# Performance work log

Hardware: AMD Instinct MI355X
Metric: run time of the kernel (lower is better)

Reference implementation:

```python
import jax, jax.numpy as jnp
import numpy as np

LAYERS = 3
DILATION = 2
RES_NORM = 1.0 / np.sqrt(2.0).astype(np.float32)
NEG_SLOPE = 0.2
T, B, D = 256, 128, 1024


def setup_inputs() -> dict:
    key = jax.random.key(0)
    k0, k1, k2, k3, k4 = jax.random.split(key, 5)
    s = 1.0 / np.sqrt(D)  # torch GRUCell default init bound
    x = jax.random.normal(k0, (1, T, B, D), dtype=jnp.float32)
    W_ih = jax.random.uniform(k1, (LAYERS, 3 * D, D), jnp.float32, -s, s)
    W_hh = jax.random.uniform(k2, (LAYERS, 3 * D, D), jnp.float32, -s, s)
    b_ih = jax.random.uniform(k3, (LAYERS, 3 * D), jnp.float32, -s, s)
    b_hh = jax.random.uniform(k4, (LAYERS, 3 * D), jnp.float32, -s, s)
    return {"x": x, "W_ih": W_ih, "W_hh": W_hh, "b_ih": b_ih, "b_hh": b_hh}


def _gru_cell(x, h, W_ih, W_hh, b_ih, b_hh):
    # torch.nn.GRUCell math
    gi = x @ W_ih.T + b_ih  # [B, 3D]
    gh = h @ W_hh.T + b_hh  # [B, 3D]
    i_r, i_z, i_n = jnp.split(gi, 3, axis=-1)
    h_r, h_z, h_n = jnp.split(gh, 3, axis=-1)
    r = jax.nn.sigmoid(i_r + h_r)
    z = jax.nn.sigmoid(i_z + h_z)
    n = jnp.tanh(i_n + r * h_n)
    return (1.0 - z) * n + z * h


def reference(x, W_ih, W_hh, b_ih, b_hh):
    xs = x[0]  # squeeze(0) -> [T, B, D]
    b, d = xs.shape[1], xs.shape[2]
    # dilated hidden buffers: layer l keeps DILATION**l past hiddens (init None -> zeros)
    bufs0 = tuple(jnp.zeros((DILATION ** l, b, d), xs.dtype) for l in range(LAYERS))

    def step(bufs, x_t):
        h_in = x_t
        new_bufs = []
        for l in range(LAYERS):
            h_out = _gru_cell(h_in, bufs[l][0], W_ih[l], W_hh[l], b_ih[l], b_hh[l])
            # append h_out, pop oldest (roll buffer)
            new_bufs.append(jnp.concatenate([bufs[l][1:], h_out[None]], axis=0))
            # layers > 1 -> dilated residual + LeakyReLU(0.2), scaled by 1/sqrt(2)
            h_in = jax.nn.leaky_relu((h_out + h_in) * RES_NORM, negative_slope=NEG_SLOPE)
        return tuple(new_bufs), h_in

    _, outs = jax.lax.scan(step, bufs0, xs)  # outs: [T, B, D]
    return outs[None]  # unsqueeze(0) -> [1, T, B, D]
```

## Files before the change

### kernel.cpp

```cpp
#include <hip/hip_runtime.h>
#include <hip/hip_bf16.h>

#define TT 256
#define D 1024
#define BD (128 * 1024)
#define NWPL 85
#define NWG 256
#define NUSED 255
#define ROWLEN 1048

typedef __attribute__((ext_vector_type(8))) short bf16x8;
typedef __attribute__((ext_vector_type(4))) float f32x4;

__device__ __forceinline__ unsigned short f2bf(float f) {
    __hip_bfloat16 h = __float2bfloat16(f);
    return *reinterpret_cast<unsigned short*>(&h);
}
__device__ __forceinline__ float bf2f(unsigned short u) {
    unsigned v = (unsigned)u << 16;
    return __builtin_bit_cast(float, v);
}

__global__ __launch_bounds__(256) void cvt_f32_bf16(const float* __restrict__ in,
                                                    unsigned short* __restrict__ out, int n) {
    int i = (blockIdx.x * 256 + threadIdx.x) * 8;
    if (i + 8 <= n) {
        float4 a = *(const float4*)(in + i);
        float4 b = *(const float4*)(in + i + 4);
        unsigned short t[8] = { f2bf(a.x), f2bf(a.y), f2bf(a.z), f2bf(a.w),
                                f2bf(b.x), f2bf(b.y), f2bf(b.z), f2bf(b.w) };
        *(uint4*)(out + i) = *(const uint4*)t;
    }
}

__global__ __launch_bounds__(256, 1) void dgru_dataflow(
    const unsigned short* __restrict__ xbf,
    const float* __restrict__ Wih, const float* __restrict__ Whh,
    const float* __restrict__ bih, const float* __restrict__ bhh,
    unsigned short* __restrict__ ring_bf, float* __restrict__ ring_f,
    unsigned short* __restrict__ hin_ring,
    float* __restrict__ out,
    unsigned* __restrict__ prog)
{
    __shared__ unsigned short wlds[78 * ROWLEN];

    const int grp = blockIdx.x & 7;
    const int p = 32 * grp + (blockIdx.x >> 3);
    if (p >= NUSED) return;
    const int layer = p / NWPL;
    const int u     = p % NWPL;
    const int ncols = (u < 4) ? 13 : 12;
    const int c0    = u * 12 + (u < 4 ? u : 4);

    {
        const float* w0 = Wih + (size_t)layer * 3 * D * D;
        const float* w1 = Whh + (size_t)layer * 3 * D * D;
        const int nrows = 6 * ncols;
        for (int rid = 0; rid < nrows; ++rid) {
            int m   = rid / (3 * ncols);
            int rem = rid - m * 3 * ncols;
            int g   = rem / ncols;
            int c   = rem - g * ncols;
            const float* src = (m ? w1 : w0) + ((size_t)g * D + c0 + c) * D + threadIdx.x * 4;
            float4 v = *(const float4*)src;
            ushort4 o = { f2bf(v.x), f2bf(v.y), f2bf(v.z), f2bf(v.w) };
            *(ushort4*)&wlds[rid * ROWLEN + threadIdx.x * 4] = o;
        }
        __syncthreads();
    }

    const int tid  = threadIdx.x;
    const int wave = tid >> 6;
    const int lane = tid & 63;
    const int r15  = lane & 15;
    const int kq   = lane >> 4;
    const int kq8  = kq * 8;
    const int c_cl = (r15 < ncols) ? r15 : (ncols - 1);
    const bool cvalid = r15 < ncols;
    const int col  = c0 + c_cl;

    const float bi2 = bih[layer * 3 * D + 2 * D + col];
    const float bh2 = bhh[layer * 3 * D + 2 * D + col];
    const float bs0 = bih[layer * 3 * D + col] + bhh[layer * 3 * D + col];
    const float bs1 = bih[layer * 3 * D + D + col] + bhh[layer * 3 * D + D + col];

    const unsigned short* bp[6];
    #pragma unroll
    for (int mg = 0; mg < 6; ++mg) bp[mg] = wlds + (mg * ncols + c_cl) * ROWLEN;

    const int arow_off0 = (wave * 32 + r15) * D;
    const int arow_off1 = (wave * 32 + 16 + r15) * D;

    const int dil = 1 << layer;
    const int R   = 2 << layer;
    const int rb  = (layer == 0) ? 0 : (layer == 1 ? 2 : 6);

    unsigned* pr0 = prog;
    unsigned* pr1 = prog + 128;
    unsigned* pr2 = prog + 256;
    unsigned* myflag = prog + layer * 128 + u;

    unsigned *a1, *a2, *a3;
    if (layer == 0)      { a1 = pr0; a2 = pr1; a3 = pr2; }
    else if (layer == 1) { a1 = pr0; a2 = pr1; a3 = pr2; }
    else                 { a1 = pr1; a2 = pr2; a3 = pr2; }

    const int j2 = (lane < 21) ? lane + 64 : lane;

    for (int t = 0; t < TT; ++t) {
        int th1, th2, th3;
        if (layer == 0)      { th1 = t;     th2 = t - 7; th3 = 0; }
        else if (layer == 1) { th1 = t + 1; th2 = t - 1; th3 = t - 7; }
        else                 { th1 = t + 1; th2 = t - 3; th3 = 0; }

        if (wave == 0) {
            for (;;) {
                bool ok = true;
                if (th1 > 0) ok = ok && (int)__hip_atomic_load(a1 + lane, __ATOMIC_RELAXED, __HIP_MEMORY_SCOPE_AGENT) >= th1
                                     && (int)__hip_atomic_load(a1 + j2,   __ATOMIC_RELAXED, __HIP_MEMORY_SCOPE_AGENT) >= th1;
                if (th2 > 0) ok = ok && (int)__hip_atomic_load(a2 + lane, __ATOMIC_RELAXED, __HIP_MEMORY_SCOPE_AGENT) >= th2
                                     && (int)__hip_atomic_load(a2 + j2,   __ATOMIC_RELAXED, __HIP_MEMORY_SCOPE_AGENT) >= th2;
                if (th3 > 0) ok = ok && (int)__hip_atomic_load(a3 + lane, __ATOMIC_RELAXED, __HIP_MEMORY_SCOPE_AGENT) >= th3
                                     && (int)__hip_atomic_load(a3 + j2,   __ATOMIC_RELAXED, __HIP_MEMORY_SCOPE_AGENT) >= th3;
                if (__all(ok)) break;
                __builtin_amdgcn_s_sleep(1);
            }
            __builtin_amdgcn_fence(__ATOMIC_ACQUIRE, "agent");
        }
        __syncthreads();

        const unsigned short* hinb = layer ? hin_ring + (size_t)((layer - 1) * 8 + (t & 7)) * BD
                                           : xbf + (size_t)t * BD;
        const int rs = (t + dil) % R, wsl = t % R;
        const unsigned short* hprevb = ring_bf + (size_t)(rb + rs) * BD;
        const float*  hprevf = ring_f + (size_t)(rb + rs) * BD;
        float*        houtf  = ring_f + (size_t)(rb + wsl) * BD;
        unsigned short* houtb = ring_bf + (size_t)(rb + wsl) * BD;

        float hpv[8], rsv[8];
        #pragma unroll
        for (int rtl = 0; rtl < 2; ++rtl)
            #pragma unroll
            for (int q = 0; q < 4; ++q) {
                const int row = wave * 32 + rtl * 16 + kq * 4 + q;
                const size_t idx = (size_t)row * D + col;
                hpv[rtl * 4 + q] = hprevf[idx];
                rsv[rtl * 4 + q] = bf2f(hinb[idx]);
            }

        f32x4 acc[2][2][3] = {};
        bf16x8 A0[16], A1[16], A2[16];

#define ISSUE1(Av, KS, SL) { \
        Av[(SL) * 4 + 0] = *(const bf16x8*)(hinb   + arow_off0 + (KS) * 32 + kq8); \
        Av[(SL) * 4 + 1] = *(const bf16x8*)(hprevb + arow_off0 + (KS) * 32 + kq8); \
        Av[(SL) * 4 + 2] = *(const bf16x8*)(hinb   + arow_off1 + (KS) * 32 + kq8); \
        Av[(SL) * 4 + 3] = *(const bf16x8*)(hprevb + arow_off1 + (KS) * 32 + kq8); }
#define ISSUEG(Av, BASE) { ISSUE1(Av, (BASE) + 0, 0) ISSUE1(Av, (BASE) + 1, 1) \
                           ISSUE1(Av, (BASE) + 2, 2) ISSUE1(Av, (BASE) + 3, 3) \
                           __builtin_amdgcn_sched_barrier(0); }
#define COMPG(Av, BASE) { _Pragma("unroll") for (int kk = 0; kk < 4; ++kk) { \
        bf16x8 Bv[6]; \
        _Pragma("unroll") for (int mg = 0; mg < 6; ++mg) \
            Bv[mg] = *(const bf16x8*)(bp[mg] + ((BASE) + kk) * 32 + kq8); \
        _Pragma("unroll") for (int g = 0; g < 3; ++g) { \
            acc[0][0][g] = __builtin_amdgcn_mfma_f32_16x16x32_bf16(Av[kk * 4 + 0], Bv[g],     acc[0][0][g], 0, 0, 0); \
            acc[0][1][g] = __builtin_amdgcn_mfma_f32_16x16x32_bf16(Av[kk * 4 + 1], Bv[3 + g], acc[0][1][g], 0, 0, 0); \
            acc[1][0][g] = __builtin_amdgcn_mfma_f32_16x16x32_bf16(Av[kk * 4 + 2], Bv[g],     acc[1][0][g], 0, 0, 0); \
            acc[1][1][g] = __builtin_amdgcn_mfma_f32_16x16x32_bf16(Av[kk * 4 + 3], Bv[3 + g], acc[1][1][g], 0, 0, 0); } } \
        __builtin_amdgcn_sched_barrier(0); }

        ISSUEG(A0, 0);  ISSUEG(A1, 4);  ISSUEG(A2, 8);
        COMPG(A0, 0);   ISSUEG(A0, 12);
        COMPG(A1, 4);   ISSUEG(A1, 16);
        COMPG(A2, 8);   ISSUEG(A2, 20);
        COMPG(A0, 12);  ISSUEG(A0, 24);
        COMPG(A1, 16);  ISSUEG(A1, 28);
        COMPG(A2, 20);
        COMPG(A0, 24);
        COMPG(A1, 28);

        #pragma unroll
        for (int rtl = 0; rtl < 2; ++rtl) {
            #pragma unroll
            for (int q = 0; q < 4; ++q) {
                const int row = wave * 32 + rtl * 16 + kq * 4 + q;
                const size_t idx = (size_t)row * D + col;
                float xr = acc[rtl][0][0][q] + acc[rtl][1][0][q] + bs0;
                float xz = acc[rtl][0][1][q] + acc[rtl][1][1][q] + bs1;
                float rg = 1.f / (1.f + __expf(-xr));
                float zg = 1.f / (1.f + __expf(-xz));
                float ng = tanhf(acc[rtl][0][2][q] + bi2 + rg * (acc[rtl][1][2][q] + bh2));
                float hp = hpv[rtl * 4 + q];
                float h  = (1.f - zg) * ng + zg * hp;
                float v = (h + rsv[rtl * 4 + q]) * 0.70710678f;
                float y = v > 0.f ? v : 0.2f * v;
                if (cvalid) {
                    __hip_atomic_store(&houtf[idx], h, __ATOMIC_RELAXED, __HIP_MEMORY_SCOPE_AGENT);
                    __hip_atomic_store(&houtb[idx], f2bf(h), __ATOMIC_RELAXED, __HIP_MEMORY_SCOPE_AGENT);
                    if (layer == 2) {
                        __hip_atomic_store(&out[(size_t)t * BD + idx], y, __ATOMIC_RELAXED, __HIP_MEMORY_SCOPE_AGENT);
                    } else {
                        __hip_atomic_store(&hin_ring[(size_t)(layer * 8 + (t & 7)) * BD + idx],
                                           f2bf(y), __ATOMIC_RELAXED, __HIP_MEMORY_SCOPE_AGENT);
                    }
                }
            }
        }

        __syncthreads();
        if (tid == 0) {
            __builtin_amdgcn_fence(__ATOMIC_RELEASE, "agent");
            __hip_atomic_store(myflag, (unsigned)(t + 1), __ATOMIC_RELAXED, __HIP_MEMORY_SCOPE_AGENT);
        }
    }
}

extern "C" void kernel_launch(void* const* d_in, const int* in_sizes, int n_in,
                              void* d_out, int out_size, void* d_ws, size_t ws_size,
                              hipStream_t stream) {
    const float* x   = (const float*)d_in[0];
    const float* Wih = (const float*)d_in[1];
    const float* Whh = (const float*)d_in[2];
    const float* bih = (const float*)d_in[3];
    const float* bhh = (const float*)d_in[4];
    float* out = (float*)d_out;

    char* ws = (char*)d_ws;
    size_t off = 0;
    auto alloc = [&](size_t bytes) -> void* {
        void* p = ws + off;
        off += (bytes + 255) & ~(size_t)255;
        return p;
    };

    const int NX = TT * BD;
    unsigned short* xbf = (unsigned short*)alloc((size_t)NX * 2);

    size_t zstart = off;
    unsigned short* ring_bf  = (unsigned short*)alloc((size_t)14 * BD * 2);
    float*          ring_f   = (float*)alloc((size_t)14 * BD * 4);
    unsigned short* hin_ring = (unsigned short*)alloc((size_t)16 * BD * 2);
    unsigned*       prog     = (unsigned*)alloc(2048);
    size_t zbytes = off - zstart;

    cvt_f32_bf16<<<NX / 8 / 256, 256, 0, stream>>>(x, xbf, NX);
    hipMemsetAsync(ws + zstart, 0, zbytes, stream);

    dgru_dataflow<<<NWG, 256, 0, stream>>>(
        xbf, Wih, Whh, bih, bhh,
        ring_bf, ring_f, hin_ring, out,
        prog);
}
```

Before: 6.001 ms.

## Restructure persistent GRU kernel to stream weights from global with LDS-staged activations

The kernel moves from 255 workgroups that each keep a bf16 weight slice resident in LDS to 96 workgroups, each owning 64 output columns by 64 batch rows of one layer. Weights are now pre-converted to bf16 once and streamed from global/L2 every timestep, while activations are staged through double-buffered LDS in 128-wide K chunks. Input x is read as fp32 and converted on the fly instead of pre-converted, and the progress-flag polling now covers 32 producers per layer. This cuts the number of synchronising blocks and the flag traffic, but each step now has to pull the full 12 MB bf16 weight set through L2 with far fewer compute units.

```diff
diff --git a/kernel.cpp b/kernel.cpp
--- a/kernel.cpp
+++ b/kernel.cpp
@@ -4,13 +4,12 @@
 #define TT 256
 #define D 1024
 #define BD (128 * 1024)
-#define NWPL 85
-#define NWG 256
-#define NUSED 255
-#define ROWLEN 1048
+#define CHUNK 128
+#define APAD 136
 
 typedef __attribute__((ext_vector_type(8))) short bf16x8;
 typedef __attribute__((ext_vector_type(4))) float f32x4;
+typedef unsigned long long ull;
 
 __device__ __forceinline__ unsigned short f2bf(float f) {
     __hip_bfloat16 h = __float2bfloat16(f);
@@ -33,185 +32,215 @@
     }
 }
 
-__global__ __launch_bounds__(256, 1) void dgru_dataflow(
-    const unsigned short* __restrict__ xbf,
-    const float* __restrict__ Wih, const float* __restrict__ Whh,
+#define MF(a, b, c) __builtin_amdgcn_mfma_f32_16x16x32_bf16(a, b, c, 0, 0, 0)
+#define SB __builtin_amdgcn_sched_barrier(0)
+#define AGLD(p) __hip_atomic_load((p), __ATOMIC_RELAXED, __HIP_MEMORY_SCOPE_AGENT)
+#define AGST(p, v) __hip_atomic_store((p), (v), __ATOMIC_RELAXED, __HIP_MEMORY_SCOPE_AGENT)
+#define LBAR { SB; asm volatile("s_waitcnt lgkmcnt(0)"); __builtin_amdgcn_s_barrier(); SB; }
+
+#define STAGE_ISSUE(KC) { \
+    if (layer == 0) { \
+        _Pragma("unroll") for (int i_ = 0; i_ < 8; ++i_) { \
+            float4 v_ = *(const float4*)(xsrc + (KC) * CHUNK + i_ * 4); \
+            Sh[i_] = (ull)f2bf(v_.x) | ((ull)f2bf(v_.y) << 16) | \
+                     ((ull)f2bf(v_.z) << 32) | ((ull)f2bf(v_.w) << 48); \
+        } \
+    } else { \
+        _Pragma("unroll") for (int i_ = 0; i_ < 8; ++i_) \
+            Sh[i_] = AGLD(hsrc + (KC) * 32 + i_); \
+    } \
+    _Pragma("unroll") for (int i_ = 0; i_ < 8; ++i_) \
+        Sp[i_] = AGLD(psrc + (KC) * 32 + i_); \
+    SB; }
+
+#define STAGE_WRITE(BUF) { \
+    _Pragma("unroll") for (int i_ = 0; i_ < 4; ++i_) { \
+        uint4 wv_; \
+        wv_.x = (unsigned)Sh[i_ * 2];     wv_.y = (unsigned)(Sh[i_ * 2] >> 32); \
+        wv_.z = (unsigned)Sh[i_ * 2 + 1]; wv_.w = (unsigned)(Sh[i_ * 2 + 1] >> 32); \
+        *(uint4*)&sA[BUF][0][srow][skp + i_ * 8] = wv_; \
+        uint4 pv_; \
+        pv_.x = (unsigned)Sp[i_ * 2];     pv_.y = (unsigned)(Sp[i_ * 2] >> 32); \
+        pv_.z = (unsigned)Sp[i_ * 2 + 1]; pv_.w = (unsigned)(Sp[i_ * 2 + 1] >> 32); \
+        *(uint4*)&sA[BUF][1][srow][skp + i_ * 8] = pv_; \
+    } SB; }
+
+#define WISSUE(W, KG) { \
+    const int ko_ = (KG) * 32; \
+    _Pragma("unroll") for (int m_ = 0; m_ < 6; ++m_) { \
+        W[m_ * 2 + 0] = *(const bf16x8*)(msrc[m_] + vcol0 + ko_); \
+        W[m_ * 2 + 1] = *(const bf16x8*)(msrc[m_] + vcol1 + ko_); \
+    } SB; }
+
+#define COMP(BUF, KSL, W) { \
+    bf16x8 a00 = *(const bf16x8*)&sA[BUF][0][wrow +  0 + r15][(KSL) * 32 + kq8]; \
+    bf16x8 a01 = *(const bf16x8*)&sA[BUF][1][wrow +  0 + r15][(KSL) * 32 + kq8]; \
+    bf16x8 a10 = *(const bf16x8*)&sA[BUF][0][wrow + 16 + r15][(KSL) * 32 + kq8]; \
+    bf16x8 a11 = *(const bf16x8*)&sA[BUF][1][wrow + 16 + r15][(KSL) * 32 + kq8]; \
+    _Pragma("unroll") for (int m_ = 0; m_ < 3; ++m_) { \
+        acc[0][0][m_] = MF(a00, W[m_ * 2 + 0], acc[0][0][m_]); \
+        acc[0][1][m_] = MF(a00, W[m_ * 2 + 1], acc[0][1][m_]); \
+        acc[1][0][m_] = MF(a10, W[m_ * 2 + 0], acc[1][0][m_]); \
+        acc[1][1][m_] = MF(a10, W[m_ * 2 + 1], acc[1][1][m_]); } \
+    _Pragma("unroll") for (int m_ = 3; m_ < 6; ++m_) { \
+        acc[0][0][m_] = MF(a01, W[m_ * 2 + 0], acc[0][0][m_]); \
+        acc[0][1][m_] = MF(a01, W[m_ * 2 + 1], acc[0][1][m_]); \
+        acc[1][0][m_] = MF(a11, W[m_ * 2 + 0], acc[1][0][m_]); \
+        acc[1][1][m_] = MF(a11, W[m_ * 2 + 1], acc[1][1][m_]); } \
+    SB; }
+
+#define EPI_ISSUE { \
+    _Pragma("unroll") for (int ct_ = 0; ct_ < 2; ++ct_) \
+    _Pragma("unroll") for (int rt_ = 0; rt_ < 2; ++rt_) \
+    _Pragma("unroll") for (int q_ = 0; q_ < 4; ++q_) { \
+        const size_t idx_ = (size_t)(rbase + wrow + rt_ * 16 + kq * 4 + q_) * D + \
+                            (c0 + wcol + ct_ * 16 + r15); \
+        hpv[ct_][rt_][q_] = AGLD(hprevf + idx_); \
+        if (layer == 0) rsl0[ct_][rt_][q_] = xt[idx_]; \
+        else rpk[ct_][rt_][q_] = AGLD((const unsigned*)(hinb + (idx_ & ~(size_t)1))); \
+    } SB; }
+
+__global__ __launch_bounds__(256, 1) void dgru3(
+    const float* __restrict__ xf,
+    const unsigned short* __restrict__ Wih_bf, const unsigned short* __restrict__ Whh_bf,
     const float* __restrict__ bih, const float* __restrict__ bhh,
     unsigned short* __restrict__ ring_bf, float* __restrict__ ring_f,
-    unsigned short* __restrict__ hin_ring,
-    float* __restrict__ out,
+    unsigned short* __restrict__ hin_ring, float* __restrict__ out,
     unsigned* __restrict__ prog)
 {
-    __shared__ unsigned short wlds[78 * ROWLEN];
-
-    const int grp = blockIdx.x & 7;
-    const int p = 32 * grp + (blockIdx.x >> 3);
-    if (p >= NUSED) return;
-    const int layer = p / NWPL;
-    const int u     = p % NWPL;
-    const int ncols = (u < 4) ? 13 : 12;
-    const int c0    = u * 12 + (u < 4 ? u : 4);
-
-    {
-        const float* w0 = Wih + (size_t)layer * 3 * D * D;
-        const float* w1 = Whh + (size_t)layer * 3 * D * D;
-        const int nrows = 6 * ncols;
-        for (int rid = 0; rid < nrows; ++rid) {
-            int m   = rid / (3 * ncols);
-            int rem = rid - m * 3 * ncols;
-            int g   = rem / ncols;
-            int c   = rem - g * ncols;
-            const float* src = (m ? w1 : w0) + ((size_t)g * D + c0 + c) * D + threadIdx.x * 4;
-            float4 v = *(const float4*)src;
-            ushort4 o = { f2bf(v.x), f2bf(v.y), f2bf(v.z), f2bf(v.w) };
-            *(ushort4*)&wlds[rid * ROWLEN + threadIdx.x * 4] = o;
-        }
-        __syncthreads();
+    __shared__ __align__(16) unsigned short sA[2][2][64][APAD];
+
+    const int b = blockIdx.x;
+    const int half  = b / 48;
+    const int p     = b % 48;
+    const int j     = p >> 3;
+    const int layer = j >> 1;
+    const int slice = (j & 1) * 8 + (p & 7);
+    const int c0    = slice * 64;
+    const int myidx = slice * 2 + half;
+    const int rbase = half * 64;
+
+    const int tid = threadIdx.x;
+    const int wave = tid >> 6, lane = tid & 63;
+    const int r15 = lane & 15, kq = lane >> 4, kq8 = kq * 8;
+    const int wrow = (wave >> 1) * 32;
+    const int wcol = (wave & 1) * 32;
+
+    const unsigned short* Wl_ih = Wih_bf + (size_t)layer * 3 * D * D;
+    const unsigned short* Wl_hh = Whh_bf + (size_t)layer * 3 * D * D;
+    const unsigned short* msrc[6] = { Wl_ih, Wl_ih + D * D, Wl_ih + 2 * D * D,
+                                      Wl_hh, Wl_hh + D * D, Wl_hh + 2 * D * D };
+    const int vcol0 = (c0 + wcol + r15) * D + kq8;
+    const int vcol1 = vcol0 + 16 * D;
+
+    float bs0[2], bs1[2], bi2c[2], bh2c[2];
+    #pragma unroll
+    for (int ct = 0; ct < 2; ++ct) {
+        const int col = c0 + wcol + ct * 16 + r15;
+        bs0[ct]  = bih[layer * 3 * D + col] + bhh[layer * 3 * D + col];
+        bs1[ct]  = bih[layer * 3 * D + D + col] + bhh[layer * 3 * D + D + col];
+        bi2c[ct] = bih[layer * 3 * D + 2 * D + col];
+        bh2c[ct] = bhh[layer * 3 * D + 2 * D + col];
     }
 
-    const int tid  = threadIdx.x;
-    const int wave = tid >> 6;
-    const int lane = tid & 63;
-    const int r15  = lane & 15;
-    const int kq   = lane >> 4;
-    const int kq8  = kq * 8;
-    const int c_cl = (r15 < ncols) ? r15 : (ncols - 1);
-    const bool cvalid = r15 < ncols;
-    const int col  = c0 + c_cl;
-
-    const float bi2 = bih[layer * 3 * D + 2 * D + col];
-    const float bh2 = bhh[layer * 3 * D + 2 * D + col];
-    const float bs0 = bih[layer * 3 * D + col] + bhh[layer * 3 * D + col];
-    const float bs1 = bih[layer * 3 * D + D + col] + bhh[layer * 3 * D + D + col];
-
-    const unsigned short* bp[6];
-    #pragma unroll
-    for (int mg = 0; mg < 6; ++mg) bp[mg] = wlds + (mg * ncols + c_cl) * ROWLEN;
-
-    const int arow_off0 = (wave * 32 + r15) * D;
-    const int arow_off1 = (wave * 32 + 16 + r15) * D;
-
-    const int dil = 1 << layer;
-    const int R   = 2 << layer;
-    const int rb  = (layer == 0) ? 0 : (layer == 1 ? 2 : 6);
+    const int srow = tid >> 2;
+    const int skp  = (tid & 3) * 32;
+    const int sgoff = (rbase + srow) * D + skp;
+
+    const int dil = 1 << layer, R = 2 << layer;
+    const int rb = (layer == 0) ? 0 : (layer == 1) ? 2 : 6;
 
     unsigned* pr0 = prog;
-    unsigned* pr1 = prog + 128;
-    unsigned* pr2 = prog + 256;
-    unsigned* myflag = prog + layer * 128 + u;
-
-    unsigned *a1, *a2, *a3;
-    if (layer == 0)      { a1 = pr0; a2 = pr1; a3 = pr2; }
-    else if (layer == 1) { a1 = pr0; a2 = pr1; a3 = pr2; }
-    else                 { a1 = pr1; a2 = pr2; a3 = pr2; }
-
-    const int j2 = (lane < 21) ? lane + 64 : lane;
+    unsigned* pr1 = prog + 64;
+    unsigned* pr2 = prog + 128;
+    unsigned* myflag = prog + layer * 64 + myidx;
+    const bool oddc = (r15 & 1);
 
     for (int t = 0; t < TT; ++t) {
-        int th1, th2, th3;
-        if (layer == 0)      { th1 = t;     th2 = t - 7; th3 = 0; }
-        else if (layer == 1) { th1 = t + 1; th2 = t - 1; th3 = t - 7; }
-        else                 { th1 = t + 1; th2 = t - 3; th3 = 0; }
-
+        int th1, th2, th3; unsigned *a1, *a2, *a3;
+        if (layer == 0)      { a1 = pr0; th1 = t;     a2 = pr1; th2 = t - 7; a3 = pr2; th3 = 0;     }
+        else if (layer == 1) { a1 = pr0; th1 = t + 1; a2 = pr1; th2 = t - 1; a3 = pr2; th3 = t - 7; }
+        else                 { a1 = pr1; th1 = t + 1; a2 = pr2; th2 = t - 3; a3 = pr2; th3 = 0;     }
         if (wave == 0) {
+            const int fi = lane & 31;
             for (;;) {
                 bool ok = true;
-                if (th1 > 0) ok = ok && (int)__hip_atomic_load(a1 + lane, __ATOMIC_RELAXED, __HIP_MEMORY_SCOPE_AGENT) >= th1
-                                     && (int)__hip_atomic_load(a1 + j2,   __ATOMIC_RELAXED, __HIP_MEMORY_SCOPE_AGENT) >= th1;
-                if (th2 > 0) ok = ok && (int)__hip_atomic_load(a2 + lane, __ATOMIC_RELAXED, __HIP_MEMORY_SCOPE_AGENT) >= th2
-                                     && (int)__hip_atomic_load(a2 + j2,   __ATOMIC_RELAXED, __HIP_MEMORY_SCOPE_AGENT) >= th2;
-                if (th3 > 0) ok = ok && (int)__hip_atomic_load(a3 + lane, __ATOMIC_RELAXED, __HIP_MEMORY_SCOPE_AGENT) >= th3
-                                     && (int)__hip_atomic_load(a3 + j2,   __ATOMIC_RELAXED, __HIP_MEMORY_SCOPE_AGENT) >= th3;
+                if (th1 > 0) ok = ok && (int)AGLD(a1 + fi) >= th1;
+                if (th2 > 0) ok = ok && (int)AGLD(a2 + fi) >= th2;
+                if (th3 > 0) ok = ok && (int)AGLD(a3 + fi) >= th3;
                 if (__all(ok)) break;
                 __builtin_amdgcn_s_sleep(1);
             }
-            __builtin_amdgcn_fence(__ATOMIC_ACQUIRE, "agent");
         }
         __syncthreads();
 
-        const unsigned short* hinb = layer ? hin_ring + (size_t)((layer - 1) * 8 + (t & 7)) * BD
-                                           : xbf + (size_t)t * BD;
+        const unsigned short* hinb = hin_ring + (size_t)((layer - 1) * 8 + (t & 7)) * BD;
+        const float* xt = xf + (size_t)t * BD;
         const int rs = (t + dil) % R, wsl = t % R;
         const unsigned short* hprevb = ring_bf + (size_t)(rb + rs) * BD;
-        const float*  hprevf = ring_f + (size_t)(rb + rs) * BD;
-        float*        houtf  = ring_f + (size_t)(rb + wsl) * BD;
+        const float* hprevf = ring_f + (size_t)(rb + rs) * BD;
+        float* houtf = ring_f + (size_t)(rb + wsl) * BD;
         unsigned short* houtb = ring_bf + (size_t)(rb + wsl) * BD;
 
-        float hpv[8], rsv[8];
+        const ull* psrc = (const ull*)(hprevb + sgoff);
+        const ull* hsrc = (layer == 0) ? (const ull*)0 : (const ull*)(hinb + sgoff);
+        const float* xsrc = xt + sgoff;
+
+        ull Sh[8], Sp[8];
+        f32x4 acc[2][2][6] = {};
+        bf16x8 W0[12], W1[12];
+        float hpv[2][2][4]; unsigned rpk[2][2][4]; float rsl0[2][2][4];
+
+        STAGE_ISSUE(0);
+        STAGE_WRITE(0); LBAR;
+        WISSUE(W0, 0);
+        #pragma unroll 1
+        for (int kc = 0; kc < 8; ++kc) {
+            const int buf = kc & 1, k4 = kc * 4;
+            if (kc < 7) { STAGE_ISSUE(kc + 1); }
+            else        { EPI_ISSUE; }
+            WISSUE(W1, k4 + 1); COMP(buf, 0, W0);
+            WISSUE(W0, k4 + 2); COMP(buf, 1, W1);
+            WISSUE(W1, k4 + 3); COMP(buf, 2, W0);
+            if (kc < 7) {
+                WISSUE(W0, k4 + 4); COMP(buf, 3, W1);
+                STAGE_WRITE(buf ^ 1); LBAR;
+            } else {
+                COMP(buf, 3, W1);
+            }
+        }
+
         #pragma unroll
-        for (int rtl = 0; rtl < 2; ++rtl)
-            #pragma unroll
-            for (int q = 0; q < 4; ++q) {
-                const int row = wave * 32 + rtl * 16 + kq * 4 + q;
-                const size_t idx = (size_t)row * D + col;
-                hpv[rtl * 4 + q] = hprevf[idx];
-                rsv[rtl * 4 + q] = bf2f(hinb[idx]);
-            }
-
-        f32x4 acc[2][2][3] = {};
-        bf16x8 A0[16], A1[16], A2[16];
-
-#define ISSUE1(Av, KS, SL) { \
-        Av[(SL) * 4 + 0] = *(const bf16x8*)(hinb   + arow_off0 + (KS) * 32 + kq8); \
-        Av[(SL) * 4 + 1] = *(const bf16x8*)(hprevb + arow_off0 + (KS) * 32 + kq8); \
-        Av[(SL) * 4 + 2] = *(const bf16x8*)(hinb   + arow_off1 + (KS) * 32 + kq8); \
-        Av[(SL) * 4 + 3] = *(const bf16x8*)(hprevb + arow_off1 + (KS) * 32 + kq8); }
-#define ISSUEG(Av, BASE) { ISSUE1(Av, (BASE) + 0, 0) ISSUE1(Av, (BASE) + 1, 1) \
-                           ISSUE1(Av, (BASE) + 2, 2) ISSUE1(Av, (BASE) + 3, 3) \
-                           __builtin_amdgcn_sched_barrier(0); }
-#define COMPG(Av, BASE) { _Pragma("unroll") for (int kk = 0; kk < 4; ++kk) { \
-        bf16x8 Bv[6]; \
-        _Pragma("unroll") for (int mg = 0; mg < 6; ++mg) \
-            Bv[mg] = *(const bf16x8*)(bp[mg] + ((BASE) + kk) * 32 + kq8); \
-        _Pragma("unroll") for (int g = 0; g < 3; ++g) { \
-            acc[0][0][g] = __builtin_amdgcn_mfma_f32_16x16x32_bf16(Av[kk * 4 + 0], Bv[g],     acc[0][0][g], 0, 0, 0); \
-            acc[0][1][g] = __builtin_amdgcn_mfma_f32_16x16x32_bf16(Av[kk * 4 + 1], Bv[3 + g], acc[0][1][g], 0, 0, 0); \
-            acc[1][0][g] = __builtin_amdgcn_mfma_f32_16x16x32_bf16(Av[kk * 4 + 2], Bv[g],     acc[1][0][g], 0, 0, 0); \
-            acc[1][1][g] = __builtin_amdgcn_mfma_f32_16x16x32_bf16(Av[kk * 4 + 3], Bv[3 + g], acc[1][1][g], 0, 0, 0); } } \
-        __builtin_amdgcn_sched_barrier(0); }
-
-        ISSUEG(A0, 0);  ISSUEG(A1, 4);  ISSUEG(A2, 8);
-        COMPG(A0, 0);   ISSUEG(A0, 12);
-        COMPG(A1, 4);   ISSUEG(A1, 16);
-        COMPG(A2, 8);   ISSUEG(A2, 20);
-        COMPG(A0, 12);  ISSUEG(A0, 24);
-        COMPG(A1, 16);  ISSUEG(A1, 28);
-        COMPG(A2, 20);
-        COMPG(A0, 24);
-        COMPG(A1, 28);
-
+        for (int ct = 0; ct < 2; ++ct)
         #pragma unroll
-        for (int rtl = 0; rtl < 2; ++rtl) {
-            #pragma unroll
-            for (int q = 0; q < 4; ++q) {
-                const int row = wave * 32 + rtl * 16 + kq * 4 + q;
-                const size_t idx = (size_t)row * D + col;
-                float xr = acc[rtl][0][0][q] + acc[rtl][1][0][q] + bs0;
-                float xz = acc[rtl][0][1][q] + acc[rtl][1][1][q] + bs1;
-                float rg = 1.f / (1.f + __expf(-xr));
-                float zg = 1.f / (1.f + __expf(-xz));
-                float ng = tanhf(acc[rtl][0][2][q] + bi2 + rg * (acc[rtl][1][2][q] + bh2));
-                float hp = hpv[rtl * 4 + q];
-                float h  = (1.f - zg) * ng + zg * hp;
-                float v = (h + rsv[rtl * 4 + q]) * 0.70710678f;
-                float y = v > 0.f ? v : 0.2f * v;
-                if (cvalid) {
-                    __hip_atomic_store(&houtf[idx], h, __ATOMIC_RELAXED, __HIP_MEMORY_SCOPE_AGENT);
-                    __hip_atomic_store(&houtb[idx], f2bf(h), __ATOMIC_RELAXED, __HIP_MEMORY_SCOPE_AGENT);
-                    if (layer == 2) {
-                        __hip_atomic_store(&out[(size_t)t * BD + idx], y, __ATOMIC_RELAXED, __HIP_MEMORY_SCOPE_AGENT);
-                    } else {
-                        __hip_atomic_store(&hin_ring[(size_t)(layer * 8 + (t & 7)) * BD + idx],
-                                           f2bf(y), __ATOMIC_RELAXED, __HIP_MEMORY_SCOPE_AGENT);
-                    }
-                }
-            }
-        }
-
+        for (int rt = 0; rt < 2; ++rt)
+        #pragma unroll
+        for (int q = 0; q < 4; ++q) {
+            const size_t idx = (size_t)(rbase + wrow + rt * 16 + kq * 4 + q) * D +
+                               (c0 + wcol + ct * 16 + r15);
+            float xr = acc[rt][ct][0][q] + acc[rt][ct][3][q] + bs0[ct];
+            float xz = acc[rt][ct][1][q] + acc[rt][ct][4][q] + bs1[ct];
+            float rg = 1.f / (1.f + __expf(-xr));
+            float zg = 1.f / (1.f + __expf(-xz));
+            float ng = tanhf(acc[rt][ct][2][q] + bi2c[ct] + rg * (acc[rt][ct][5][q] + bh2c[ct]));
+            float hp = hpv[ct][rt][q];
+            float h  = (1.f - zg) * ng + zg * hp;
+            float res = (layer == 0) ? rsl0[ct][rt][q]
+                        : bf2f((unsigned short)(oddc ? (rpk[ct][rt][q] >> 16)
+                                                     : (rpk[ct][rt][q] & 0xffffu)));
+            float v = (h + res) * 0.70710678f;
+            float y = v > 0.f ? v : 0.2f * v;
+            AGST(&houtf[idx], h);
+            AGST(&houtb[idx], f2bf(h));
+            if (layer == 2) AGST(&out[(size_t)t * BD + idx], y);
+            else            AGST(&hin_ring[(size_t)(layer * 8 + (t & 7)) * BD + idx], f2bf(y));
+        }
+
+        asm volatile("s_waitcnt vmcnt(0)");
         __syncthreads();
         if (tid == 0) {
             __builtin_amdgcn_fence(__ATOMIC_RELEASE, "agent");
-            __hip_atomic_store(myflag, (unsigned)(t + 1), __ATOMIC_RELAXED, __HIP_MEMORY_SCOPE_AGENT);
+            AGST(myflag, (unsigned)(t + 1));
         }
     }
 }
@@ -234,21 +263,22 @@
         return p;
     };
 
-    const int NX = TT * BD;
-    unsigned short* xbf = (unsigned short*)alloc((size_t)NX * 2);
+    const int nW = 3 * 3 * D * D;
+    unsigned short* Wih_bf = (unsigned short*)alloc((size_t)nW * 2);
+    unsigned short* Whh_bf = (unsigned short*)alloc((size_t)nW * 2);
 
     size_t zstart = off;
     unsigned short* ring_bf  = (unsigned short*)alloc((size_t)14 * BD * 2);
     float*          ring_f   = (float*)alloc((size_t)14 * BD * 4);
     unsigned short* hin_ring = (unsigned short*)alloc((size_t)16 * BD * 2);
-    unsigned*       prog     = (unsigned*)alloc(2048);
+    unsigned*       prog     = (unsigned*)alloc(1024);
     size_t zbytes = off - zstart;
 
-    cvt_f32_bf16<<<NX / 8 / 256, 256, 0, stream>>>(x, xbf, NX);
+    cvt_f32_bf16<<<nW / 8 / 256, 256, 0, stream>>>(Wih, Wih_bf, nW);
+    cvt_f32_bf16<<<nW / 8 / 256, 256, 0, stream>>>(Whh, Whh_bf, nW);
     hipMemsetAsync(ws + zstart, 0, zbytes, stream);
 
-    dgru_dataflow<<<NWG, 256, 0, stream>>>(
-        xbf, Wih, Whh, bih, bhh,
-        ring_bf, ring_f, hin_ring, out,
-        prog);
-}
+    dgru3<<<96, 256, 0, stream>>>(
+        x, Wih_bf, Whh_bf, bih, bhh,
+        ring_bf, ring_f, hin_ring, out, prog);
+}
```

After: 19.89 ms. 3.31x slower.
